# Optimization experiments

Hardware: AMD Instinct MI355X
Metric: run time of the kernel (lower is better)

Reference implementation:

```python
import jax, jax.numpy as jnp
import numpy as np

B, C, IMG, P = 64, 3, 224, 16
D, L, H, DH, M, NC = 768, 12, 12, 64, 3072, 1000
INNER = H * DH
PD = C * P * P          # patch_dim = 768
NP = (IMG // P) ** 2    # 196 patches


def setup_inputs() -> dict:
    key = jax.random.key(0)
    ks = jax.random.split(key, 16)
    s = 0.02
    nrm = lambda k, shape: jax.random.normal(k, shape, jnp.float32) * s
    return dict(
        img=jax.random.normal(ks[0], (B, C, IMG, IMG), jnp.float32),
        patch_ln1_g=jnp.ones(PD), patch_ln1_b=jnp.zeros(PD),
        patch_w=nrm(ks[1], (PD, D)), patch_b=jnp.zeros(D),
        patch_ln2_g=jnp.ones(D), patch_ln2_b=jnp.zeros(D),
        pos_emb=nrm(ks[2], (1, NP + 1, D)),
        cls_tok=nrm(ks[3], (1, 1, D)),
        attn_ln_g=jnp.ones((L, D)), attn_ln_b=jnp.zeros((L, D)),
        w_qkv=nrm(ks[4], (L, D, 3 * INNER)),
        w_out=nrm(ks[5], (L, INNER, D)), b_out=jnp.zeros((L, D)),
        ff_ln_g=jnp.ones((L, D)), ff_ln_b=jnp.zeros((L, D)),
        ff_w1=nrm(ks[6], (L, D, M)), ff_b1=jnp.zeros((L, M)),
        ff_w2=nrm(ks[7], (L, M, D)), ff_b2=jnp.zeros((L, D)),
        final_ln_g=jnp.ones(D), final_ln_b=jnp.zeros(D),
        head_w=nrm(ks[8], (D, NC)), head_b=jnp.zeros(NC),
    )


def _ln(x, g, b, eps=1e-5):
    m = x.mean(-1, keepdims=True)
    v = ((x - m) ** 2).mean(-1, keepdims=True)
    return (x - m) / jnp.sqrt(v + eps) * g + b


def reference(img, patch_ln1_g, patch_ln1_b, patch_w, patch_b, patch_ln2_g,
              patch_ln2_b, pos_emb, cls_tok, attn_ln_g, attn_ln_b, w_qkv,
              w_out, b_out, ff_ln_g, ff_ln_b, ff_w1, ff_b1, ff_w2, ff_b2,
              final_ln_g, final_ln_b, head_w, head_b):
    b, c, hh, ww = img.shape
    h, w = hh // P, ww // P
    # Rearrange 'b c (h p1) (w p2) -> b (h w) (p1 p2 c)'
    x = img.reshape(b, c, h, P, w, P).transpose(0, 2, 4, 3, 5, 1).reshape(b, h * w, P * P * c)
    x = _ln(x, patch_ln1_g, patch_ln1_b)
    x = x @ patch_w + patch_b
    x = _ln(x, patch_ln2_g, patch_ln2_b)
    n = x.shape[1]
    x = jnp.concatenate([jnp.broadcast_to(cls_tok, (b, 1, x.shape[-1])), x], axis=1)
    x = x + pos_emb[:, : n + 1]
    scale = DH ** -0.5
    for l in range(L):
        xn = _ln(x, attn_ln_g[l], attn_ln_b[l])
        qkv = xn @ w_qkv[l]  # [b, n+1, 3*inner]
        q, k, v = jnp.split(qkv, 3, axis=-1)
        sp = lambda t: t.reshape(b, -1, H, DH).transpose(0, 2, 1, 3)  # b h n d
        q, k, v = sp(q), sp(k), sp(v)
        # softmax variant: exp(scores*scale), normalize by sum + eps (no max-subtract, faithful to source)
        numer = jnp.exp(jnp.einsum('bhid,bhjd->bhij', q, k) * scale)
        attn = numer / (numer.sum(-1, keepdims=True) + 1e-8)
        out = jnp.einsum('bhij,bhjd->bhid', attn, v)
        out = out.transpose(0, 2, 1, 3).reshape(b, -1, INNER)
        x = out @ w_out[l] + b_out[l] + x
        xn = _ln(x, ff_ln_g[l], ff_ln_b[l])
        hid = jax.nn.gelu(xn @ ff_w1[l] + ff_b1[l], approximate=False)
        x = hid @ ff_w2[l] + ff_b2[l] + x
    x = _ln(x, final_ln_g, final_ln_b)
    return x[:, 0] @ head_w + head_b
```

## Files before the change

kernel.cpp:

```cpp
#include <hip/hip_runtime.h>
#include <hip/hip_bf16.h>
#include <math.h>

#define B_     64
#define NTOK   197
#define NPATCH 196
#define D768   768
#define NL     12
#define NH     12
#define MFF    3072
#define NCLS   1000
#define ROWS   (B_ * NTOK)
#define PROWS  (B_ * NPATCH)
#define ROWS_PAD 12672

typedef unsigned short ushort;
typedef __bf16 bf16x8 __attribute__((ext_vector_type(8)));
typedef float  f32x4  __attribute__((ext_vector_type(4)));
typedef unsigned short u16x4 __attribute__((ext_vector_type(4)));

__device__ __forceinline__ ushort f2b(float f) {
  __hip_bfloat16 h = __float2bfloat16(f);
  return *reinterpret_cast<ushort*>(&h);
}

__device__ __forceinline__ void gload16(const ushort* g, ushort* lds) {
  __builtin_amdgcn_global_load_lds((const __attribute__((address_space(1))) void*)g,
                                   (__attribute__((address_space(3))) void*)lds, 16, 0, 0);
}

__device__ __forceinline__ void block_mean_rstd(float s, float sq, float& mean, float& rstd) {
#pragma unroll
  for (int off = 32; off; off >>= 1) { s += __shfl_xor(s, off); sq += __shfl_xor(sq, off); }
  __shared__ float ss[4], ssq[4];
  int w = threadIdx.x >> 6;
  if ((threadIdx.x & 63) == 0) { ss[w] = s; ssq[w] = sq; }
  __syncthreads();
  s  = ss[0] + ss[1] + ss[2] + ss[3];
  sq = ssq[0] + ssq[1] + ssq[2] + ssq[3];
  mean = s * (1.0f / 768.0f);
  float var = sq * (1.0f / 768.0f) - mean * mean;
  rstd = rsqrtf(var + 1e-5f);
}

__global__ __launch_bounds__(256) void ln_rows_b(const float* __restrict__ in, long in_stride,
                                                 const float* __restrict__ g,
                                                 const float* __restrict__ bta,
                                                 ushort* __restrict__ out) {
  const float* xr = in + (size_t)blockIdx.x * in_stride;
  int t = threadIdx.x;
  float v0 = xr[t], v1 = xr[t + 256], v2 = xr[t + 512];
  float mean, rstd;
  block_mean_rstd(v0 + v1 + v2, v0 * v0 + v1 * v1 + v2 * v2, mean, rstd);
  ushort* o = out + (size_t)blockIdx.x * 768;
  o[t]       = f2b((v0 - mean) * rstd * g[t]       + bta[t]);
  o[t + 256] = f2b((v1 - mean) * rstd * g[t + 256] + bta[t + 256]);
  o[t + 512] = f2b((v2 - mean) * rstd * g[t + 512] + bta[t + 512]);
}

__global__ __launch_bounds__(256) void patch_ln1(const float* __restrict__ img,
                                                 const float* __restrict__ g,
                                                 const float* __restrict__ bta,
                                                 ushort* __restrict__ xp) {
  int pidx = blockIdx.x;
  int b = pidx / NPATCH, hw = pidx % NPATCH;
  int ph = hw / 14, pw = hw % 14;
  int t = threadIdx.x;
  float v[3];
#pragma unroll
  for (int u = 0; u < 3; ++u) {
    int k = t + u * 256;
    int c = k % 3, p2 = (k / 3) & 15, p1 = k / 48;
    v[u] = img[(((size_t)b * 3 + c) * 224 + ph * 16 + p1) * 224 + pw * 16 + p2];
  }
  float mean, rstd;
  block_mean_rstd(v[0] + v[1] + v[2], v[0] * v[0] + v[1] * v[1] + v[2] * v[2], mean, rstd);
  ushort* o = xp + (size_t)pidx * 768;
#pragma unroll
  for (int u = 0; u < 3; ++u) { int k = t + u * 256; o[k] = f2b((v[u] - mean) * rstd * g[k] + bta[k]); }
}

__global__ __launch_bounds__(256) void ln2_pos(const float* __restrict__ xe,
                                               const float* __restrict__ g,
                                               const float* __restrict__ bta,
                                               const float* __restrict__ pos,
                                               float* __restrict__ x) {
  int pidx = blockIdx.x;
  int b = pidx / NPATCH, i = pidx % NPATCH;
  const float* xr = xe + (size_t)pidx * 768;
  int t = threadIdx.x;
  float v0 = xr[t], v1 = xr[t + 256], v2 = xr[t + 512];
  float mean, rstd;
  block_mean_rstd(v0 + v1 + v2, v0 * v0 + v1 * v1 + v2 * v2, mean, rstd);
  const float* p = pos + (size_t)(1 + i) * 768;
  float* o = x + ((size_t)b * NTOK + 1 + i) * 768;
  o[t]       = (v0 - mean) * rstd * g[t]       + bta[t]       + p[t];
  o[t + 256] = (v1 - mean) * rstd * g[t + 256] + bta[t + 256] + p[t + 256];
  o[t + 512] = (v2 - mean) * rstd * g[t + 512] + bta[t + 512] + p[t + 512];
}

__global__ __launch_bounds__(256) void cls_init(const float* __restrict__ cls_tok,
                                                const float* __restrict__ pos,
                                                float* __restrict__ x) {
  int b = blockIdx.x, t = threadIdx.x;
  float* o = x + (size_t)b * NTOK * 768;
#pragma unroll
  for (int u = 0; u < 3; ++u) { int k = t + u * 256; o[k] = cls_tok[k] + pos[k]; }
}

__global__ __launch_bounds__(256) void transpose_cast(const float* __restrict__ W,
                                                      ushort* __restrict__ Wt,
                                                      int K, int N) {
  __shared__ float t[32][33];
  int n0 = blockIdx.x * 32, k0 = blockIdx.y * 32;
  int tx = threadIdx.x, ty = threadIdx.y;
#pragma unroll
  for (int u = 0; u < 32; u += 8) {
    int n = n0 + tx;
    t[ty + u][tx] = (n < N) ? W[(size_t)(k0 + ty + u) * N + n] : 0.f;
  }
  __syncthreads();
#pragma unroll
  for (int u = 0; u < 32; u += 8) {
    int n = n0 + ty + u;
    if (n < N) Wt[(size_t)n * K + k0 + tx] = f2b(t[tx][ty + u]);
  }
}

__global__ __launch_bounds__(256) void transpose4(const float* __restrict__ wq,
                                                  const float* __restrict__ wo,
                                                  const float* __restrict__ w1,
                                                  const float* __restrict__ w2,
                                                  ushort* __restrict__ tq,
                                                  ushort* __restrict__ to,
                                                  ushort* __restrict__ t1,
                                                  ushort* __restrict__ t2) {
  int bid = blockIdx.x;
  const float* W; ushort* Wt; int K, N, xt;
  if (bid < 1728)      {             W = wq; Wt = tq; K = 768;  N = 2304; xt = 72; }
  else if (bid < 2304) { bid -= 1728; W = wo; Wt = to; K = 768;  N = 768;  xt = 24; }
  else if (bid < 4608) { bid -= 2304; W = w1; Wt = t1; K = 768;  N = 3072; xt = 96; }
  else                 { bid -= 4608; W = w2; Wt = t2; K = 3072; N = 768;  xt = 24; }
  int n0 = (bid % xt) * 32, k0 = (bid / xt) * 32;
  __shared__ float t[32][33];
  int tx = threadIdx.x, ty = threadIdx.y;
#pragma unroll
  for (int u = 0; u < 32; u += 8)
    t[ty + u][tx] = W[(size_t)(k0 + ty + u) * N + n0 + tx];
  __syncthreads();
#pragma unroll
  for (int u = 0; u < 32; u += 8)
    Wt[(size_t)(n0 + ty + u) * K + k0 + tx] = f2b(t[tx][ty + u]);
}

template<int EP, int RESID, int OBF>
__global__ __launch_bounds__(256) void gemm_v3(const ushort* __restrict__ A,
                                               const ushort* __restrict__ Bt,
                                               const float* __restrict__ bias,
                                               const float* __restrict__ resid,
                                               void* __restrict__ Cv,
                                               int M, int N, int K) {
  __shared__ ushort smem[2 * 16384];

  const int tid = threadIdx.x;
  const int w = tid >> 6, l = tid & 63;
  const int fr = l & 15, fc = l >> 4;

  const int ntx = gridDim.x;
  const int nwg = ntx * gridDim.y;
  const int orig = blockIdx.y * ntx + blockIdx.x;
  const int q = nwg >> 3, r = nwg & 7, xcd = orig & 7, idx = orig >> 3;
  const int wg = (xcd < r ? xcd * (q + 1) : r * (q + 1) + (xcd - r) * q) + idx;
  const int row0 = (wg / ntx) * 128, col0 = (wg % ntx) * 128;

  const int wr = (w >> 1) * 64, wc = (w & 1) * 64;

  const int srow = w * 8 + (l >> 3);
  const int sg = (l & 7) ^ (l >> 3);
  const ushort* pA[4]; const ushort* pB[4];
#pragma unroll
  for (int i = 0; i < 4; ++i) {
    pA[i] = A  + (size_t)(row0 + i * 32 + srow) * K + sg * 8;
    pB[i] = Bt + (size_t)(col0 + i * 32 + srow) * K + sg * 8;
  }

  auto stage = [&](int k0, int buf) {
    ushort* As = smem + buf * 16384;
    ushort* Bs = As + 8192;
#pragma unroll
    for (int i = 0; i < 4; ++i) {
      gload16(pA[i] + k0, As + (i * 256 + w * 64) * 8);
      gload16(pB[i] + k0, Bs + (i * 256 + w * 64) * 8);
    }
  };

  f32x4 acc[4][4] = {};
  const int nIter = K >> 6;

  stage(0, 0);
  asm volatile("s_waitcnt vmcnt(0)" ::: "memory");
  __builtin_amdgcn_s_barrier();

  int buf = 0;
  for (int t = 0; t < nIter; ++t) {
    if (t + 1 < nIter) stage((t + 1) * 64, buf ^ 1);
    const ushort* As = smem + buf * 16384;
    const ushort* Bs = As + 8192;
#pragma unroll
    for (int ks = 0; ks < 2; ++ks) {
      const int sw = ((ks * 4 + fc) ^ (fr & 7)) << 3;
      bf16x8 a_[4], b_[4];
#pragma unroll
      for (int m = 0; m < 4; ++m)
        a_[m] = *(const bf16x8*)(As + (wr + m * 16 + fr) * 64 + sw);
#pragma unroll
      for (int n = 0; n < 4; ++n)
        b_[n] = *(const bf16x8*)(Bs + (wc + n * 16 + fr) * 64 + sw);
#pragma unroll
      for (int m = 0; m < 4; ++m)
#pragma unroll
        for (int n = 0; n < 4; ++n)
          acc[m][n] = __builtin_amdgcn_mfma_f32_16x16x32_bf16(b_[n], a_[m], acc[m][n], 0, 0, 0);
    }
    asm volatile("s_waitcnt vmcnt(0)" ::: "memory");
    __builtin_amdgcn_s_barrier();
    buf ^= 1;
  }

  if (!OBF) {
    float* Cf = (float*)Cv;
#pragma unroll
    for (int m = 0; m < 4; ++m) {
      int row = row0 + wr + m * 16 + fr;
      if (row >= M) continue;
#pragma unroll
      for (int n = 0; n < 4; ++n) {
        int col = col0 + wc + n * 16 + fc * 4;
        f32x4 v = acc[m][n];
        if (bias) v += *(const f32x4*)(bias + col);
        if (EP) {
#pragma unroll
          for (int rr = 0; rr < 4; ++rr)
            v[rr] = 0.5f * v[rr] * (1.0f + erff(v[rr] * 0.70710678118654752f));
        }
        if (RESID) v += *(const f32x4*)(resid + (size_t)row * N + col);
        *(f32x4*)(Cf + (size_t)row * N + col) = v;
      }
    }
  } else {
    ushort* Cw = smem + w * 4096;
#pragma unroll
    for (int m = 0; m < 4; ++m) {
      int rl = m * 16 + fr;
#pragma unroll
      for (int n = 0; n < 4; ++n) {
        int col = col0 + wc + n * 16 + fc * 4;
        f32x4 v = acc[m][n];
        if (bias) v += *(const f32x4*)(bias + col);
        if (EP) {
#pragma unroll
          for (int rr = 0; rr < 4; ++rr)
            v[rr] = 0.5f * v[rr] * (1.0f + erff(v[rr] * 0.70710678118654752f));
        }
        u16x4 pk = { f2b(v[0]), f2b(v[1]), f2b(v[2]), f2b(v[3]) };
        int s = (n * 4 + fc) ^ (rl & 7);
        *(u16x4*)(Cw + rl * 64 + s * 4) = pk;
      }
    }
    ushort* Cb = (ushort*)Cv;
#pragma unroll
    for (int pp = 0; pp < 16; ++pp) {
      int rl = pp * 4 + (l >> 4);
      int cs = l & 15;
      u16x4 pk = *(const u16x4*)(Cw + rl * 64 + ((cs ^ (rl & 7)) * 4));
      int row = row0 + wr + rl;
      if (row < M) *(u16x4*)(Cb + (size_t)row * N + col0 + wc + cs * 4) = pk;
    }
  }
}

template<int EP, int RESID, int OBF>
__global__ __launch_bounds__(256) void gemm_bt(const ushort* __restrict__ A,
                                               const ushort* __restrict__ Bt,
                                               const float* __restrict__ bias,
                                               const float* __restrict__ resid,
                                               void* __restrict__ C,
                                               int M, int N, int K) {
  __shared__ ushort As[128 * 32];
  __shared__ ushort Bs[128 * 32];
  int tid = threadIdx.x;
  int w = tid >> 6, l = tid & 63;
  int fr = l & 15, fc = l >> 4;
  int row0 = blockIdx.y * 128, col0 = blockIdx.x * 128;
  int wr = (w >> 1) * 64, wc = (w & 1) * 64;

  int srow0 = w * 32 + (l >> 2);
  int srow1 = srow0 + 16;
  int sc0 = (((l & 3) ^ ((srow0 >> 1) & 3)) << 3);
  int sc1 = (((l & 3) ^ ((srow1 >> 1) & 3)) << 3);
  const ushort* ga0 = A  + (size_t)(row0 + srow0) * K + sc0;
  const ushort* ga1 = A  + (size_t)(row0 + srow1) * K + sc1;
  const ushort* gb0 = Bt + (size_t)(col0 + srow0) * K + sc0;
  const ushort* gb1 = Bt + (size_t)(col0 + srow1) * K + sc1;

  int idxA[4], idxB[4];
#pragma unroll
  for (int m = 0; m < 4; ++m) {
    int rA = wr + m * 16 + fr;
    idxA[m] = rA * 32 + ((fc ^ ((rA >> 1) & 3)) << 3);
  }
#pragma unroll
  for (int n = 0; n < 4; ++n) {
    int rB = wc + n * 16 + fr;
    idxB[n] = rB * 32 + ((fc ^ ((rB >> 1) & 3)) << 3);
  }

  f32x4 acc[4][4] = {};

  for (int k0 = 0; k0 < K; k0 += 32) {
    gload16(ga0 + k0, &As[w * 1024]);
    gload16(ga1 + k0, &As[w * 1024 + 512]);
    gload16(gb0 + k0, &Bs[w * 1024]);
    gload16(gb1 + k0, &Bs[w * 1024 + 512]);
    __syncthreads();
    bf16x8 af[4], bfr[4];
#pragma unroll
    for (int m = 0; m < 4; ++m) af[m] = *(const bf16x8*)(As + idxA[m]);
#pragma unroll
    for (int n = 0; n < 4; ++n) bfr[n] = *(const bf16x8*)(Bs + idxB[n]);
#pragma unroll
    for (int m = 0; m < 4; ++m)
#pragma unroll
      for (int n = 0; n < 4; ++n)
        acc[m][n] = __builtin_amdgcn_mfma_f32_16x16x32_bf16(af[m], bfr[n], acc[m][n], 0, 0, 0);
    __syncthreads();
  }

#pragma unroll
  for (int n = 0; n < 4; ++n) {
    int col = col0 + wc + n * 16 + fr;
    if (col >= N) continue;
    float bv = bias ? bias[col] : 0.f;
#pragma unroll
    for (int m = 0; m < 4; ++m) {
#pragma unroll
      for (int rr = 0; rr < 4; ++rr) {
        int row = row0 + wr + m * 16 + fc * 4 + rr;
        if (row >= M) continue;
        float v = acc[m][n][rr] + bv;
        if (EP == 1) v = 0.5f * v * (1.0f + erff(v * 0.70710678118654752f));
        if (RESID) v += resid[(size_t)row * N + col];
        if (OBF) ((ushort*)C)[(size_t)row * N + col] = f2b(v);
        else     ((float*)C)[(size_t)row * N + col]  = v;
      }
    }
  }
}

__global__ __launch_bounds__(256) void attn_mfma(const ushort* __restrict__ qkv,
                                                 ushort* __restrict__ aout) {
  int bid = blockIdx.x;
  int qt = bid & 3;
  int h  = (bid >> 2) % NH;
  int b  = (bid >> 2) / NH;
  int tid = threadIdx.x, w = tid >> 6, l = tid & 63;
  int fr = l & 15, fc = l >> 4;

  __shared__ ushort Vt[64 * 64];
  __shared__ ushort Pl[4 * 16 * 64];

  const size_t brow = (size_t)b * NTOK;
  int q0 = qt * 64 + w * 16;

  bf16x8 qf[2];
  {
    const ushort* qp = qkv + (brow + q0 + fr) * 2304 + h * 64 + fc * 8;
    qf[0] = *(const bf16x8*)qp;
    qf[1] = *(const bf16x8*)(qp + 32);
  }
  float rs[4] = {0.f, 0.f, 0.f, 0.f};
  f32x4 oc[4] = {};

  for (int kt = 0; kt < 4; ++kt) {
    __syncthreads();
    {
      int key = tid >> 2, d0 = (tid & 3) * 16;
      int j = kt * 64 + key;
      bool valid = j < NTOK;
      const ushort* vp = qkv + (brow + j) * 2304 + 1536 + h * 64 + d0;
      ushort vbuf[16];
      if (valid) {
        *(bf16x8*)(vbuf)     = *(const bf16x8*)vp;
        *(bf16x8*)(vbuf + 8) = *(const bf16x8*)(vp + 8);
      } else {
#pragma unroll
        for (int i = 0; i < 16; ++i) vbuf[i] = 0;
      }
#pragma unroll
      for (int i = 0; i < 16; ++i) {
        int d = d0 + i;
        int byte = d * 128 + ((((key >> 3)) ^ (d & 7)) << 4) + (key & 7) * 2;
        Vt[byte >> 1] = vbuf[i];
      }
    }
    f32x4 sc[4];
#pragma unroll
    for (int n = 0; n < 4; ++n) {
      f32x4 z = {};
      const ushort* kp = qkv + (brow + kt * 64 + n * 16 + fr) * 2304 + 768 + h * 64 + fc * 8;
      bf16x8 k0 = *(const bf16x8*)kp;
      bf16x8 k1 = *(const bf16x8*)(kp + 32);
      z = __builtin_amdgcn_mfma_f32_16x16x32_bf16(qf[0], k0, z, 0, 0, 0);
      z = __builtin_amdgcn_mfma_f32_16x16x32_bf16(qf[1], k1, z, 0, 0, 0);
      sc[n] = z;
    }
    float part[4] = {0.f, 0.f, 0.f, 0.f};
#pragma unroll
    for (int n = 0; n < 4; ++n) {
      int j = kt * 64 + n * 16 + fr;
      bool jv = j < NTOK;
#pragma unroll
      for (int rr = 0; rr < 4; ++rr) {
        float e = jv ? __expf(sc[n][rr] * 0.125f) : 0.f;
        part[rr] += e;
        int row = fc * 4 + rr, col = n * 16 + fr;
        int byte = row * 128 + (((col >> 3) ^ (row & 7)) << 4) + (col & 7) * 2;
        Pl[w * 1024 + (byte >> 1)] = f2b(e);
      }
    }
#pragma unroll
    for (int rr = 0; rr < 4; ++rr) {
      float p = part[rr];
      p += __shfl_xor(p, 1); p += __shfl_xor(p, 2);
      p += __shfl_xor(p, 4); p += __shfl_xor(p, 8);
      rs[rr] += p;
    }
    __syncthreads();
#pragma unroll
    for (int ks = 0; ks < 2; ++ks) {
      int prow = fr;
      int pbyte = prow * 128 + (((ks * 4 + fc) ^ (prow & 7)) << 4);
      bf16x8 pf = *(const bf16x8*)(Pl + w * 1024 + (pbyte >> 1));
#pragma unroll
      for (int n = 0; n < 4; ++n) {
        int d = n * 16 + fr;
        int vb = d * 128 + (((ks * 4 + fc) ^ (d & 7)) << 4);
        bf16x8 vf = *(const bf16x8*)(Vt + (vb >> 1));
        oc[n] = __builtin_amdgcn_mfma_f32_16x16x32_bf16(pf, vf, oc[n], 0, 0, 0);
      }
    }
  }
#pragma unroll
  for (int n = 0; n < 4; ++n) {
#pragma unroll
    for (int rr = 0; rr < 4; ++rr) {
      int qq = q0 + fc * 4 + rr;
      if (qq < NTOK) {
        float v = oc[n][rr] / (rs[rr] + 1e-8f);
        aout[(brow + qq) * 768 + h * 64 + n * 16 + fr] = f2b(v);
      }
    }
  }
}

extern "C" void kernel_launch(void* const* d_in, const int* in_sizes, int n_in,
                              void* d_out, int out_size, void* d_ws, size_t ws_size,
                              hipStream_t stream) {
  const float* img       = (const float*)d_in[0];
  const float* p_ln1_g   = (const float*)d_in[1];
  const float* p_ln1_b   = (const float*)d_in[2];
  const float* patch_w   = (const float*)d_in[3];
  const float* patch_b   = (const float*)d_in[4];
  const float* p_ln2_g   = (const float*)d_in[5];
  const float* p_ln2_b   = (const float*)d_in[6];
  const float* pos_emb   = (const float*)d_in[7];
  const float* cls_tok   = (const float*)d_in[8];
  const float* attn_ln_g = (const float*)d_in[9];
  const float* attn_ln_b = (const float*)d_in[10];
  const float* w_qkv     = (const float*)d_in[11];
  const float* w_out     = (const float*)d_in[12];
  const float* b_out     = (const float*)d_in[13];
  const float* ff_ln_g   = (const float*)d_in[14];
  const float* ff_ln_b   = (const float*)d_in[15];
  const float* ff_w1     = (const float*)d_in[16];
  const float* ff_b1     = (const float*)d_in[17];
  const float* ff_w2     = (const float*)d_in[18];
  const float* ff_b2     = (const float*)d_in[19];
  const float* fin_ln_g  = (const float*)d_in[20];
  const float* fin_ln_b  = (const float*)d_in[21];
  const float* head_w    = (const float*)d_in[22];
  const float* head_b    = (const float*)d_in[23];
  float* out = (float*)d_out;

  char* p = (char*)d_ws;
  auto alloc = [&](size_t bytes) { char* r = p; p += (bytes + 255) & ~(size_t)255; return r; };
  float*  x      = (float*) alloc((size_t)ROWS_PAD * 768 * 4);
  ushort* xnb    = (ushort*)alloc((size_t)ROWS_PAD * 768 * 2);
  ushort* qkvb   = (ushort*)alloc((size_t)ROWS_PAD * 2304 * 2);
  ushort* aoutb  = (ushort*)alloc((size_t)ROWS_PAD * 768 * 2);
  ushort* wtq    = (ushort*)alloc((size_t)2304 * 768 * 2);
  ushort* wto    = (ushort*)alloc((size_t)768 * 768 * 2);
  ushort* wt1    = (ushort*)alloc((size_t)3072 * 768 * 2);
  ushort* wt2    = (ushort*)alloc((size_t)768 * 3072 * 2);
  ushort* pwt    = (ushort*)alloc((size_t)768 * 768 * 2);
  ushort* hwt    = (ushort*)alloc((size_t)1024 * 768 * 2);
  ushort* xclsb  = (ushort*)alloc((size_t)128 * 768 * 2);
  ushort* hidb   = qkvb;
  ushort* xpb    = xnb;
  float*  xe     = (float*)qkvb;

  dim3 blk(256), tblk(32, 8);

  transpose_cast<<<dim3(24, 24), tblk, 0, stream>>>(patch_w, pwt, 768, 768);
  transpose_cast<<<dim3(32, 24), tblk, 0, stream>>>(head_w, hwt, 768, 1000);
  patch_ln1<<<PROWS, blk, 0, stream>>>(img, p_ln1_g, p_ln1_b, xpb);
  gemm_v3<0, 0, 0><<<dim3(6, 98), blk, 0, stream>>>(xpb, pwt, patch_b, nullptr, xe,
                                                    PROWS, 768, 768);
  ln2_pos<<<PROWS, blk, 0, stream>>>(xe, p_ln2_g, p_ln2_b, pos_emb, x);
  cls_init<<<B_, blk, 0, stream>>>(cls_tok, pos_emb, x);

  for (int l = 0; l < NL; ++l) {
    transpose4<<<6912, tblk, 0, stream>>>(w_qkv + (size_t)l * 768 * 2304,
                                          w_out + (size_t)l * 768 * 768,
                                          ff_w1 + (size_t)l * 768 * MFF,
                                          ff_w2 + (size_t)l * MFF * 768,
                                          wtq, wto, wt1, wt2);

    ln_rows_b<<<ROWS, blk, 0, stream>>>(x, 768, attn_ln_g + (size_t)l * 768,
                                        attn_ln_b + (size_t)l * 768, xnb);
    gemm_v3<0, 0, 1><<<dim3(18, 99), blk, 0, stream>>>(xnb, wtq, nullptr, nullptr, qkvb,
                                                       ROWS, 2304, 768);
    attn_mfma<<<B_ * NH * 4, blk, 0, stream>>>(qkvb, aoutb);
    gemm_v3<0, 1, 0><<<dim3(6, 99), blk, 0, stream>>>(aoutb, wto, b_out + (size_t)l * 768,
                                                      x, x, ROWS, 768, 768);
    ln_rows_b<<<ROWS, blk, 0, stream>>>(x, 768, ff_ln_g + (size_t)l * 768,
                                        ff_ln_b + (size_t)l * 768, xnb);
    gemm_v3<1, 0, 1><<<dim3(24, 99), blk, 0, stream>>>(xnb, wt1, ff_b1 + (size_t)l * MFF,
                                                       nullptr, hidb, ROWS, MFF, 768);
    gemm_v3<0, 1, 0><<<dim3(6, 99), blk, 0, stream>>>(hidb, wt2, ff_b2 + (size_t)l * 768,
                                                      x, x, ROWS, 768, MFF);
  }

  ln_rows_b<<<B_, blk, 0, stream>>>(x, (long)NTOK * 768, fin_ln_g, fin_ln_b, xclsb);
  gemm_bt<0, 0, 0><<<dim3(8, 1), blk, 0, stream>>>(xclsb, hwt, head_b, nullptr, out,
                                                   B_, NCLS, 768);
}
```

Baseline: 4.546 ms.

## Use triple-buffered K=32 LDS pipeline in GEMM and tanh-approx GELU

The GEMM main loop moves from a double-buffered 64-wide K step to a three-stage ring of 32-wide K tiles. Two tiles stay in flight, waited on with a partial vmcnt, and the swizzle pattern and LDS index precomputation are changed to match the new tile width. The exact erf GELU in the FFN epilogue becomes a tanh-style approximation written as a sigmoid with __expf, which is cheaper but slightly less accurate. LDS use drops from 64KB to 48KB, which may allow more resident blocks, at the cost of more barriers per K.

After: 4.424 ms. 1.03x faster.

```diff
diff --git a/kernel.cpp b/kernel.cpp
--- a/kernel.cpp
+++ b/kernel.cpp
@@ -27,6 +27,11 @@
 __device__ __forceinline__ void gload16(const ushort* g, ushort* lds) {
   __builtin_amdgcn_global_load_lds((const __attribute__((address_space(1))) void*)g,
                                    (__attribute__((address_space(3))) void*)lds, 16, 0, 0);
+}
+
+__device__ __forceinline__ float gelu_f(float v) {
+  float t = v * fmaf(0.0713548162726f, v * v, 1.5957691216f);
+  return v / (1.0f + __expf(-t));
 }
 
 __device__ __forceinline__ void block_mean_rstd(float s, float sq, float& mean, float& rstd) {
@@ -154,13 +159,13 @@
 }
 
 template<int EP, int RESID, int OBF>
-__global__ __launch_bounds__(256) void gemm_v3(const ushort* __restrict__ A,
+__global__ __launch_bounds__(256) void gemm_v4(const ushort* __restrict__ A,
                                                const ushort* __restrict__ Bt,
                                                const float* __restrict__ bias,
                                                const float* __restrict__ resid,
                                                void* __restrict__ Cv,
                                                int M, int N, int K) {
-  __shared__ ushort smem[2 * 16384];
+  __shared__ ushort smem[3 * 8192];
 
   const int tid = threadIdx.x;
   const int w = tid >> 6, l = tid & 63;
@@ -175,56 +180,65 @@
 
   const int wr = (w >> 1) * 64, wc = (w & 1) * 64;
 
-  const int srow = w * 8 + (l >> 3);
-  const int sg = (l & 7) ^ (l >> 3);
-  const ushort* pA[4]; const ushort* pB[4];
-#pragma unroll
-  for (int i = 0; i < 4; ++i) {
-    pA[i] = A  + (size_t)(row0 + i * 32 + srow) * K + sg * 8;
-    pB[i] = Bt + (size_t)(col0 + i * 32 + srow) * K + sg * 8;
-  }
-
-  auto stage = [&](int k0, int buf) {
-    ushort* As = smem + buf * 16384;
-    ushort* Bs = As + 8192;
-#pragma unroll
-    for (int i = 0; i < 4; ++i) {
-      gload16(pA[i] + k0, As + (i * 256 + w * 64) * 8);
-      gload16(pB[i] + k0, Bs + (i * 256 + w * 64) * 8);
-    }
+  const int srow = tid >> 2;
+  const int sg = (tid & 3) ^ ((srow >> 1) & 3);
+  const ushort* pA0 = A  + (size_t)(row0 + srow) * K + sg * 8;
+  const ushort* pA1 = A  + (size_t)(row0 + 64 + srow) * K + sg * 8;
+  const ushort* pB0 = Bt + (size_t)(col0 + srow) * K + sg * 8;
+  const ushort* pB1 = Bt + (size_t)(col0 + 64 + srow) * K + sg * 8;
+
+  auto stage = [&](int t_, int bi_) {
+    ushort* dst = smem + bi_ * 8192;
+    const int k0 = t_ * 32;
+    gload16(pA0 + k0, dst + tid * 8);
+    gload16(pA1 + k0, dst + (tid + 256) * 8);
+    gload16(pB0 + k0, dst + 4096 + tid * 8);
+    gload16(pB1 + k0, dst + 4096 + (tid + 256) * 8);
   };
 
+  int idxA[4], idxB[4];
+#pragma unroll
+  for (int m = 0; m < 4; ++m) {
+    int rA = wr + m * 16 + fr;
+    idxA[m] = rA * 32 + ((fc ^ ((rA >> 1) & 3)) << 3);
+  }
+#pragma unroll
+  for (int n = 0; n < 4; ++n) {
+    int rB = wc + n * 16 + fr;
+    idxB[n] = rB * 32 + ((fc ^ ((rB >> 1) & 3)) << 3);
+  }
+
   f32x4 acc[4][4] = {};
-  const int nIter = K >> 6;
+  const int NT = K >> 5;
 
   stage(0, 0);
-  asm volatile("s_waitcnt vmcnt(0)" ::: "memory");
+  stage(1, 1);
+  asm volatile("s_waitcnt vmcnt(4)" ::: "memory");
   __builtin_amdgcn_s_barrier();
 
-  int buf = 0;
-  for (int t = 0; t < nIter; ++t) {
-    if (t + 1 < nIter) stage((t + 1) * 64, buf ^ 1);
-    const ushort* As = smem + buf * 16384;
-    const ushort* Bs = As + 8192;
-#pragma unroll
-    for (int ks = 0; ks < 2; ++ks) {
-      const int sw = ((ks * 4 + fc) ^ (fr & 7)) << 3;
-      bf16x8 a_[4], b_[4];
-#pragma unroll
-      for (int m = 0; m < 4; ++m)
-        a_[m] = *(const bf16x8*)(As + (wr + m * 16 + fr) * 64 + sw);
+  int bi = 0, si = 2;
+  for (int t = 0; t < NT; ++t) {
+    const bool more2 = (t + 2 < NT);
+    if (more2) stage(t + 2, si);
+    const ushort* As = smem + bi * 8192;
+    const ushort* Bs = As + 4096;
+    bf16x8 a_[4], b_[4];
+#pragma unroll
+    for (int m = 0; m < 4; ++m) a_[m] = *(const bf16x8*)(As + idxA[m]);
+#pragma unroll
+    for (int n = 0; n < 4; ++n) b_[n] = *(const bf16x8*)(Bs + idxB[n]);
+#pragma unroll
+    for (int m = 0; m < 4; ++m)
 #pragma unroll
       for (int n = 0; n < 4; ++n)
-        b_[n] = *(const bf16x8*)(Bs + (wc + n * 16 + fr) * 64 + sw);
-#pragma unroll
-      for (int m = 0; m < 4; ++m)
-#pragma unroll
-        for (int n = 0; n < 4; ++n)
-          acc[m][n] = __builtin_amdgcn_mfma_f32_16x16x32_bf16(b_[n], a_[m], acc[m][n], 0, 0, 0);
-    }
-    asm volatile("s_waitcnt vmcnt(0)" ::: "memory");
-    __builtin_amdgcn_s_barrier();
-    buf ^= 1;
+        acc[m][n] = __builtin_amdgcn_mfma_f32_16x16x32_bf16(b_[n], a_[m], acc[m][n], 0, 0, 0);
+    if (t + 1 < NT) {
+      if (more2) asm volatile("s_waitcnt vmcnt(4)" ::: "memory");
+      else       asm volatile("s_waitcnt vmcnt(0)" ::: "memory");
+      __builtin_amdgcn_s_barrier();
+    }
+    bi = (bi == 2) ? 0 : bi + 1;
+    si = (si == 2) ? 0 : si + 1;
   }
 
   if (!OBF) {
@@ -240,14 +254,14 @@
         if (bias) v += *(const f32x4*)(bias + col);
         if (EP) {
 #pragma unroll
-          for (int rr = 0; rr < 4; ++rr)
-            v[rr] = 0.5f * v[rr] * (1.0f + erff(v[rr] * 0.70710678118654752f));
+          for (int rr = 0; rr < 4; ++rr) v[rr] = gelu_f(v[rr]);
         }
         if (RESID) v += *(const f32x4*)(resid + (size_t)row * N + col);
         *(f32x4*)(Cf + (size_t)row * N + col) = v;
       }
     }
   } else {
+    __syncthreads();
     ushort* Cw = smem + w * 4096;
 #pragma unroll
     for (int m = 0; m < 4; ++m) {
@@ -259,8 +273,7 @@
         if (bias) v += *(const f32x4*)(bias + col);
         if (EP) {
 #pragma unroll
-          for (int rr = 0; rr < 4; ++rr)
-            v[rr] = 0.5f * v[rr] * (1.0f + erff(v[rr] * 0.70710678118654752f));
+          for (int rr = 0; rr < 4; ++rr) v[rr] = gelu_f(v[rr]);
         }
         u16x4 pk = { f2b(v[0]), f2b(v[1]), f2b(v[2]), f2b(v[3]) };
         int s = (n * 4 + fc) ^ (rl & 7);
@@ -514,7 +527,7 @@
   transpose_cast<<<dim3(24, 24), tblk, 0, stream>>>(patch_w, pwt, 768, 768);
   transpose_cast<<<dim3(32, 24), tblk, 0, stream>>>(head_w, hwt, 768, 1000);
   patch_ln1<<<PROWS, blk, 0, stream>>>(img, p_ln1_g, p_ln1_b, xpb);
-  gemm_v3<0, 0, 0><<<dim3(6, 98), blk, 0, stream>>>(xpb, pwt, patch_b, nullptr, xe,
+  gemm_v4<0, 0, 0><<<dim3(6, 98), blk, 0, stream>>>(xpb, pwt, patch_b, nullptr, xe,
                                                     PROWS, 768, 768);
   ln2_pos<<<PROWS, blk, 0, stream>>>(xe, p_ln2_g, p_ln2_b, pos_emb, x);
   cls_init<<<B_, blk, 0, stream>>>(cls_tok, pos_emb, x);
@@ -528,16 +541,16 @@
 
     ln_rows_b<<<ROWS, blk, 0, stream>>>(x, 768, attn_ln_g + (size_t)l * 768,
                                         attn_ln_b + (size_t)l * 768, xnb);
-    gemm_v3<0, 0, 1><<<dim3(18, 99), blk, 0, stream>>>(xnb, wtq, nullptr, nullptr, qkvb,
+    gemm_v4<0, 0, 1><<<dim3(18, 99), blk, 0, stream>>>(xnb, wtq, nullptr, nullptr, qkvb,
                                                        ROWS, 2304, 768);
     attn_mfma<<<B_ * NH * 4, blk, 0, stream>>>(qkvb, aoutb);
-    gemm_v3<0, 1, 0><<<dim3(6, 99), blk, 0, stream>>>(aoutb, wto, b_out + (size_t)l * 768,
+    gemm_v4<0, 1, 0><<<dim3(6, 99), blk, 0, stream>>>(aoutb, wto, b_out + (size_t)l * 768,
                                                       x, x, ROWS, 768, 768);
     ln_rows_b<<<ROWS, blk, 0, stream>>>(x, 768, ff_ln_g + (size_t)l * 768,
                                         ff_ln_b + (size_t)l * 768, xnb);
-    gemm_v3<1, 0, 1><<<dim3(24, 99), blk, 0, stream>>>(xnb, wt1, ff_b1 + (size_t)l * MFF,
+    gemm_v4<1, 0, 1><<<dim3(24, 99), blk, 0, stream>>>(xnb, wt1, ff_b1 + (size_t)l * MFF,
                                                        nullptr, hidb, ROWS, MFF, 768);
-    gemm_v3<0, 1, 0><<<dim3(6, 99), blk, 0, stream>>>(hidb, wt2, ff_b2 + (size_t)l * 768,
+    gemm_v4<0, 1, 0><<<dim3(6, 99), blk, 0, stream>>>(hidb, wt2, ff_b2 + (size_t)l * 768,
                                                       x, x, ROWS, 768, MFF);
   }
 
```
